# Optimization experiments

Hardware: AMD Instinct MI355X
Metric: run time of the kernel (lower is better)

## Reference

```python
import jax, jax.numpy as jnp
import numpy as np

N, B, D, Q = 32, 36, 2048, 1024  # batch, objects, v_dim, q_dim


def setup_inputs() -> dict:
    key = jax.random.key(0)
    ks = jax.random.split(key, 6)
    sc = 0.02  # small init so ReLU chains stay well-scaled
    return {
        "v": jax.random.normal(ks[0], (N, B, D), jnp.float32),
        "q": jax.random.normal(ks[1], (N, Q), jnp.float32),
        "W1": jax.random.normal(ks[2], (D, D), jnp.float32) * sc,
        "b1": jnp.zeros((D,), jnp.float32),
        "W2": jax.random.normal(ks[3], (D, D), jnp.float32) * sc,
        "b2": jnp.zeros((D,), jnp.float32),
        "W3": jax.random.normal(ks[4], (Q, D), jnp.float32) * sc,
        "b3": jnp.zeros((D,), jnp.float32),
    }


def reference(v, q, W1, b1, W2, b2, W3, b3):
    # FCNet = ReLU(Linear(.)) with weight-norm folded, dropout=0 (eval).
    # Original calls linear3 twice (linear4 unused bug), so q_emb == q_emb2.
    qe = jax.nn.relu(q @ W3 + b3)  # (N, D)
    # pairs[n,i,j] = v[n,i]*qe[n] + v[n,j]*qe[n]  -> (N, B, B, D)
    pairs = (v[:, :, None, :] + v[:, None, :, :]) * qe[:, None, None, :]
    h = jax.nn.relu(jnp.einsum('nijd,de->nije', pairs, W1) + b1)  # linear1
    x = jnp.sum(h, axis=2)  # sum over j relations -> (N, B, D)
    return jax.nn.relu(x @ W2 + b2)  # linear2
```

## Files before the change

kernel.cpp:

```cpp
#include <hip/hip_runtime.h>
#include <stdint.h>

#define N_BATCH 32
#define B_OBJ   36
#define D_DIM   2048
#define Q_DIM   1024

typedef __bf16 bf16x8 __attribute__((ext_vector_type(8)));
typedef float  f32x4  __attribute__((ext_vector_type(4)));

__device__ __forceinline__ uint16_t f2bf(float f) {
    uint32_t u = __builtin_bit_cast(uint32_t, f);
    uint32_t r = (u + 0x7FFFu + ((u >> 16) & 1u)) >> 16;
    return (uint16_t)r;
}

__device__ __forceinline__ void gld_lds16(const void* g, void* l) {
    __builtin_amdgcn_global_load_lds(
        (const __attribute__((address_space(1))) uint32_t*)g,
        (__attribute__((address_space(3))) uint32_t*)l, 16, 0, 0);
}

__global__ __launch_bounds__(256) void transpose_all(
    const float* __restrict__ W1, const float* __restrict__ W2,
    const float* __restrict__ W3,
    uint16_t* __restrict__ W1t, uint16_t* __restrict__ W2t,
    uint16_t* __restrict__ W3t) {
    __shared__ float tile[64][65];
    int gy = blockIdx.y;
    const float* W; uint16_t* Wt; int K, k0;
    if (gy < 32)      { W = W1; Wt = W1t; K = 2048; k0 = gy * 64; }
    else if (gy < 64) { W = W2; Wt = W2t; K = 2048; k0 = (gy - 32) * 64; }
    else              { W = W3; Wt = W3t; K = 1024; k0 = (gy - 64) * 64; }
    int n0 = blockIdx.x * 64;
    int t = threadIdx.x;
    {
        int r = t >> 4, c = (t & 15) * 4;
#pragma unroll
        for (int p = 0; p < 4; ++p)
            *(float4*)&tile[r + p * 16][c] =
                *(const float4*)&W[(size_t)(k0 + r + p * 16) * 2048 + n0 + c];
    }
    __syncthreads();
    {
        int n = t >> 2, kb = (t & 3) * 16;
#pragma unroll
        for (int g4 = 0; g4 < 4; ++g4) {
            int k = kb + g4 * 4;
            ushort4 o;
            o.x = f2bf(tile[k][n]);     o.y = f2bf(tile[k + 1][n]);
            o.z = f2bf(tile[k + 2][n]); o.w = f2bf(tile[k + 3][n]);
            *(ushort4*)&Wt[(size_t)(n0 + n) * K + k0 + k] = o;
        }
    }
}

__global__ __launch_bounds__(256) void qk_gemm(
    const float* __restrict__ q,
    const uint16_t* __restrict__ W3t,
    float* __restrict__ qpart) {
    __shared__ __align__(16) uint16_t As[32][32];
    __shared__ __align__(16) uint16_t Bs[128][32];
    int t = threadIdx.x, lane = t & 63, wave = t >> 6;
    int l15 = lane & 15, quad = lane >> 4;
    int n0 = blockIdx.x * 128;
    int kbase = blockIdx.y * 256;
    f32x4 acc[2][2] = {};
    int ar = t >> 3, ac = (t & 7) * 4;
    int br = t >> 2, bk = (t & 3) * 8;

    for (int k0 = 0; k0 < 256; k0 += 32) {
        __syncthreads();
        float4 av = *(const float4*)&q[(size_t)ar * Q_DIM + kbase + k0 + ac];
        ushort4 a4;
        a4.x = f2bf(av.x); a4.y = f2bf(av.y); a4.z = f2bf(av.z); a4.w = f2bf(av.w);
        *(ushort4*)&As[ar][ac] = a4;
        *(uint4*)&Bs[br][bk]      = *(const uint4*)&W3t[(size_t)(n0 + br) * Q_DIM + kbase + k0 + bk];
        *(uint4*)&Bs[br + 64][bk] = *(const uint4*)&W3t[(size_t)(n0 + br + 64) * Q_DIM + kbase + k0 + bk];
        __syncthreads();
        bf16x8 af[2], bfr[2];
        af[0]  = *(const bf16x8*)&As[l15][quad * 8];
        af[1]  = *(const bf16x8*)&As[16 + l15][quad * 8];
        bfr[0] = *(const bf16x8*)&Bs[wave * 32 + l15][quad * 8];
        bfr[1] = *(const bf16x8*)&Bs[wave * 32 + 16 + l15][quad * 8];
#pragma unroll
        for (int i = 0; i < 2; ++i)
#pragma unroll
            for (int j = 0; j < 2; ++j)
                acc[i][j] = __builtin_amdgcn_mfma_f32_16x16x32_bf16(af[i], bfr[j], acc[i][j], 0, 0, 0);
    }
    float* dst = qpart + (size_t)blockIdx.y * 32 * D_DIM;
#pragma unroll
    for (int i = 0; i < 2; ++i)
#pragma unroll
        for (int j = 0; j < 2; ++j) {
            int n = n0 + wave * 32 + j * 16 + l15;
#pragma unroll
            for (int r = 0; r < 4; ++r)
                dst[(size_t)(i * 16 + quad * 4 + r) * D_DIM + n] = acc[i][j][r];
        }
}

__global__ __launch_bounds__(128) void qe_make_u(
    const float* __restrict__ qpart, const float* __restrict__ b3,
    const float* __restrict__ v, uint16_t* __restrict__ u) {
    int nb = blockIdx.y;
    int d4 = blockIdx.x * 128 + threadIdx.x;
    const float4* p = (const float4*)qpart;
    size_t base = (size_t)nb * 512 + d4;
    float4 s0 = p[base], s1 = p[16384 + base], s2 = p[32768 + base], s3 = p[49152 + base];
    float4 b = ((const float4*)b3)[d4];
    float4 qe;
    qe.x = fmaxf(s0.x + s1.x + s2.x + s3.x + b.x, 0.f);
    qe.y = fmaxf(s0.y + s1.y + s2.y + s3.y + b.y, 0.f);
    qe.z = fmaxf(s0.z + s1.z + s2.z + s3.z + b.z, 0.f);
    qe.w = fmaxf(s0.w + s1.w + s2.w + s3.w + b.w, 0.f);
    const float4* v4 = (const float4*)v;
    ushort4* u4 = (ushort4*)u;
    size_t rb = (size_t)nb * B_OBJ * 512 + d4;
#pragma unroll 4
    for (int i = 0; i < B_OBJ; ++i) {
        float4 vv = v4[rb + (size_t)i * 512];
        ushort4 o;
        o.x = f2bf(vv.x * qe.x);
        o.y = f2bf(vv.y * qe.y);
        o.z = f2bf(vv.z * qe.z);
        o.w = f2bf(vv.w * qe.w);
        u4[rb + (size_t)i * 512] = o;
    }
}

__global__ __launch_bounds__(512) void gemm_batch(
    const uint16_t* __restrict__ A,
    const uint16_t* __restrict__ Bt,
    const float* __restrict__ bias,
    void* __restrict__ Cv,
    int mode) {
    __shared__ __align__(16) uint16_t smem[2][14336];
    float* yt = (float*)&smem[0][0];

    int t = threadIdx.x, lane = t & 63, wave = t >> 6;
    int l15 = lane & 15, quad = lane >> 4;
    int wr = wave >> 2, wc = wave & 3;
    int nbp = blockIdx.y;
    int n0 = blockIdx.x * 128;
    const uint16_t* Ab = A + (size_t)nbp * 72 * D_DIM;

    const uint16_t* gp[4];
    int loff[4];
    int wslot = (lane & 3) ^ ((lane >> 2) & 3);
#pragma unroll
    for (int c = 0; c < 4; ++c) {
        int r = wave + 8 * c;
        int rr = (r < 28) ? r : 0;
        if (rr < 12) {
            int g = rr >> 1, h = rr & 1;
            int arow = g * 16 + (lane >> 2) - (g >= 3 ? 12 : 0);
            gp[c] = Ab + (size_t)arow * D_DIM + h * 32 + wslot * 8;
            loff[c] = h * 3072 + g * 512;
        } else {
            int rb = rr - 12, g = rb >> 1, h = rb & 1;
            int brow = g * 16 + (lane >> 2);
            gp[c] = Bt + (size_t)(n0 + brow) * D_DIM + h * 32 + wslot * 8;
            loff[c] = 6144 + h * 4096 + g * 512;
        }
    }

    f32x4 acc[3][2] = {};
    int rslot = quad ^ (l15 & 3);

#define STAGE(kk, bi)                                    \
    {                                                    \
        _Pragma("unroll")                                \
        for (int c = 0; c < 4; ++c)                      \
            if (wave + 8 * c < 28)                       \
                gld_lds16(gp[c] + (kk), &smem[bi][loff[c]]); \
    }
#define WAIT_L()                                                      \
    {                                                                 \
        if (wave < 4) asm volatile("s_waitcnt vmcnt(4)" ::: "memory");\
        else          asm volatile("s_waitcnt vmcnt(3)" ::: "memory");\
    }

    STAGE(0, 0);
    STAGE(64, 1);
    WAIT_L();
    __builtin_amdgcn_s_barrier();

    for (int k = 0; k < 32; ++k) {
        int cur = k & 1;
        const uint16_t* As = &smem[cur][0];
        const uint16_t* Bs = As + 6144;
#pragma unroll
        for (int s = 0; s < 2; ++s) {
            bf16x8 af[3], bfr[2];
#pragma unroll
            for (int i = 0; i < 3; ++i)
                af[i] = *(const bf16x8*)(As + s * 3072 + (wr * 48 + i * 16 + l15) * 32 + rslot * 8);
#pragma unroll
            for (int j = 0; j < 2; ++j)
                bfr[j] = *(const bf16x8*)(Bs + s * 4096 + (wc * 32 + j * 16 + l15) * 32 + rslot * 8);
#pragma unroll
            for (int i = 0; i < 3; ++i)
#pragma unroll
                for (int j = 0; j < 2; ++j)
                    acc[i][j] = __builtin_amdgcn_mfma_f32_16x16x32_bf16(af[i], bfr[j], acc[i][j], 0, 0, 0);
        }
        if (k == 31) break;
        __builtin_amdgcn_s_barrier();
        if (k < 30) {
            STAGE((k + 2) * 64, cur);
            WAIT_L();
        } else {
            asm volatile("s_waitcnt vmcnt(0)" ::: "memory");
        }
        __builtin_amdgcn_s_barrier();
    }
#undef STAGE
#undef WAIT_L

    if (mode == 0) {
        uint16_t* X = (uint16_t*)Cv;
        __syncthreads();
#pragma unroll
        for (int i = 0; i < 3; ++i)
#pragma unroll
            for (int j = 0; j < 2; ++j)
#pragma unroll
                for (int r = 0; r < 4; ++r)
                    yt[(wr * 48 + i * 16 + quad * 4 + r) * 132 + wc * 32 + j * 16 + l15] = acc[i][j][r];
        __syncthreads();
        int col = t & 127, sub = t >> 7;
        int b = sub >> 1, half = sub & 1;
        float bv = bias[n0 + col];
        float z[36];
#pragma unroll
        for (int j = 0; j < 36; ++j) z[j] = yt[(b * 48 + j) * 132 + col];
#pragma unroll
        for (int ii = 0; ii < 18; ++ii) {
            int i = half * 18 + ii;
            float zi = z[i] + bv;
            float s = 0.f;
#pragma unroll
            for (int j = 0; j < 36; ++j) s += fmaxf(zi + z[j], 0.f);
            X[(size_t)((nbp * 2 + b) * B_OBJ + i) * D_DIM + n0 + col] = f2bf(s);
        }
    } else {
        float* O = (float*)Cv;
#pragma unroll
        for (int i = 0; i < 3; ++i)
#pragma unroll
            for (int r = 0; r < 4; ++r) {
                int obj = i * 16 + quad * 4 + r;
                if (obj < B_OBJ) {
#pragma unroll
                    for (int j = 0; j < 2; ++j) {
                        int cc = n0 + wc * 32 + j * 16 + l15;
                        O[(size_t)((nbp * 2 + wr) * B_OBJ + obj) * D_DIM + cc] =
                            fmaxf(acc[i][j][r] + bias[cc], 0.f);
                    }
                }
            }
    }
}

extern "C" void kernel_launch(void* const* d_in, const int* in_sizes, int n_in,
                              void* d_out, int out_size, void* d_ws, size_t ws_size,
                              hipStream_t stream) {
    const float* v  = (const float*)d_in[0];
    const float* q  = (const float*)d_in[1];
    const float* W1 = (const float*)d_in[2];
    const float* b1 = (const float*)d_in[3];
    const float* W2 = (const float*)d_in[4];
    const float* b2 = (const float*)d_in[5];
    const float* W3 = (const float*)d_in[6];
    const float* b3 = (const float*)d_in[7];
    float* out = (float*)d_out;

    char* ws = (char*)d_ws;
    uint16_t* W1t   = (uint16_t*)(ws + 0);
    uint16_t* W2t   = (uint16_t*)(ws + 8388608);
    uint16_t* W3t   = (uint16_t*)(ws + 16777216);
    uint16_t* u     = (uint16_t*)(ws + 16777216);
    float*    qpart = (float*)   (ws + 21495808);
    uint16_t* x     = (uint16_t*)(ws + 22806528);

    transpose_all<<<dim3(32, 80), 256, 0, stream>>>(W1, W2, W3, W1t, W2t, W3t);

    qk_gemm<<<dim3(16, 4), 256, 0, stream>>>(q, W3t, qpart);

    qe_make_u<<<dim3(4, N_BATCH), 128, 0, stream>>>(qpart, b3, v, u);

    gemm_batch<<<dim3(16, 16), 512, 0, stream>>>(u, W1t, b1, x, 0);

    gemm_batch<<<dim3(16, 16), 512, 0, stream>>>(x, W2t, b2, out, 1);
}
```

Baseline: 171.9 us.

## Fuse all five stages into one cooperative persistent kernel with grid syncs

Replaces the five separate launches (weight transpose/convert, q GEMM, qe/u build, and two batched GEMMs) with one cooperative kernel of 256 blocks. Grid-wide barriers separate the stages. The weight transpose runs as a grid-stride loop, with two 256-thread halves per block each using their own shared-memory tile. The goal is to remove per-launch overhead and the idle gaps between kernels. In exchange it adds grid.sync costs and fixes the grid at 256×512 threads for every phase, so the small stages leave most blocks idle.

Result: slower. 305.7 us (+77.8%).

```diff
diff --git a/kernel.cpp b/kernel.cpp
--- a/kernel.cpp
+++ b/kernel.cpp
@@ -1,5 +1,8 @@
 #include <hip/hip_runtime.h>
+#include <hip/hip_cooperative_groups.h>
 #include <stdint.h>
+
+namespace cg = cooperative_groups;
 
 #define N_BATCH 32
 #define B_OBJ   36
@@ -21,129 +24,16 @@
         (__attribute__((address_space(3))) uint32_t*)l, 16, 0, 0);
 }
 
-__global__ __launch_bounds__(256) void transpose_all(
-    const float* __restrict__ W1, const float* __restrict__ W2,
-    const float* __restrict__ W3,
-    uint16_t* __restrict__ W1t, uint16_t* __restrict__ W2t,
-    uint16_t* __restrict__ W3t) {
-    __shared__ float tile[64][65];
-    int gy = blockIdx.y;
-    const float* W; uint16_t* Wt; int K, k0;
-    if (gy < 32)      { W = W1; Wt = W1t; K = 2048; k0 = gy * 64; }
-    else if (gy < 64) { W = W2; Wt = W2t; K = 2048; k0 = (gy - 32) * 64; }
-    else              { W = W3; Wt = W3t; K = 1024; k0 = (gy - 64) * 64; }
-    int n0 = blockIdx.x * 64;
-    int t = threadIdx.x;
-    {
-        int r = t >> 4, c = (t & 15) * 4;
-#pragma unroll
-        for (int p = 0; p < 4; ++p)
-            *(float4*)&tile[r + p * 16][c] =
-                *(const float4*)&W[(size_t)(k0 + r + p * 16) * 2048 + n0 + c];
-    }
-    __syncthreads();
-    {
-        int n = t >> 2, kb = (t & 3) * 16;
-#pragma unroll
-        for (int g4 = 0; g4 < 4; ++g4) {
-            int k = kb + g4 * 4;
-            ushort4 o;
-            o.x = f2bf(tile[k][n]);     o.y = f2bf(tile[k + 1][n]);
-            o.z = f2bf(tile[k + 2][n]); o.w = f2bf(tile[k + 3][n]);
-            *(ushort4*)&Wt[(size_t)(n0 + n) * K + k0 + k] = o;
-        }
-    }
-}
-
-__global__ __launch_bounds__(256) void qk_gemm(
-    const float* __restrict__ q,
-    const uint16_t* __restrict__ W3t,
-    float* __restrict__ qpart) {
-    __shared__ __align__(16) uint16_t As[32][32];
-    __shared__ __align__(16) uint16_t Bs[128][32];
-    int t = threadIdx.x, lane = t & 63, wave = t >> 6;
-    int l15 = lane & 15, quad = lane >> 4;
-    int n0 = blockIdx.x * 128;
-    int kbase = blockIdx.y * 256;
-    f32x4 acc[2][2] = {};
-    int ar = t >> 3, ac = (t & 7) * 4;
-    int br = t >> 2, bk = (t & 3) * 8;
-
-    for (int k0 = 0; k0 < 256; k0 += 32) {
-        __syncthreads();
-        float4 av = *(const float4*)&q[(size_t)ar * Q_DIM + kbase + k0 + ac];
-        ushort4 a4;
-        a4.x = f2bf(av.x); a4.y = f2bf(av.y); a4.z = f2bf(av.z); a4.w = f2bf(av.w);
-        *(ushort4*)&As[ar][ac] = a4;
-        *(uint4*)&Bs[br][bk]      = *(const uint4*)&W3t[(size_t)(n0 + br) * Q_DIM + kbase + k0 + bk];
-        *(uint4*)&Bs[br + 64][bk] = *(const uint4*)&W3t[(size_t)(n0 + br + 64) * Q_DIM + kbase + k0 + bk];
-        __syncthreads();
-        bf16x8 af[2], bfr[2];
-        af[0]  = *(const bf16x8*)&As[l15][quad * 8];
-        af[1]  = *(const bf16x8*)&As[16 + l15][quad * 8];
-        bfr[0] = *(const bf16x8*)&Bs[wave * 32 + l15][quad * 8];
-        bfr[1] = *(const bf16x8*)&Bs[wave * 32 + 16 + l15][quad * 8];
-#pragma unroll
-        for (int i = 0; i < 2; ++i)
-#pragma unroll
-            for (int j = 0; j < 2; ++j)
-                acc[i][j] = __builtin_amdgcn_mfma_f32_16x16x32_bf16(af[i], bfr[j], acc[i][j], 0, 0, 0);
-    }
-    float* dst = qpart + (size_t)blockIdx.y * 32 * D_DIM;
-#pragma unroll
-    for (int i = 0; i < 2; ++i)
-#pragma unroll
-        for (int j = 0; j < 2; ++j) {
-            int n = n0 + wave * 32 + j * 16 + l15;
-#pragma unroll
-            for (int r = 0; r < 4; ++r)
-                dst[(size_t)(i * 16 + quad * 4 + r) * D_DIM + n] = acc[i][j][r];
-        }
-}
-
-__global__ __launch_bounds__(128) void qe_make_u(
-    const float* __restrict__ qpart, const float* __restrict__ b3,
-    const float* __restrict__ v, uint16_t* __restrict__ u) {
-    int nb = blockIdx.y;
-    int d4 = blockIdx.x * 128 + threadIdx.x;
-    const float4* p = (const float4*)qpart;
-    size_t base = (size_t)nb * 512 + d4;
-    float4 s0 = p[base], s1 = p[16384 + base], s2 = p[32768 + base], s3 = p[49152 + base];
-    float4 b = ((const float4*)b3)[d4];
-    float4 qe;
-    qe.x = fmaxf(s0.x + s1.x + s2.x + s3.x + b.x, 0.f);
-    qe.y = fmaxf(s0.y + s1.y + s2.y + s3.y + b.y, 0.f);
-    qe.z = fmaxf(s0.z + s1.z + s2.z + s3.z + b.z, 0.f);
-    qe.w = fmaxf(s0.w + s1.w + s2.w + s3.w + b.w, 0.f);
-    const float4* v4 = (const float4*)v;
-    ushort4* u4 = (ushort4*)u;
-    size_t rb = (size_t)nb * B_OBJ * 512 + d4;
-#pragma unroll 4
-    for (int i = 0; i < B_OBJ; ++i) {
-        float4 vv = v4[rb + (size_t)i * 512];
-        ushort4 o;
-        o.x = f2bf(vv.x * qe.x);
-        o.y = f2bf(vv.y * qe.y);
-        o.z = f2bf(vv.z * qe.z);
-        o.w = f2bf(vv.w * qe.w);
-        u4[rb + (size_t)i * 512] = o;
-    }
-}
-
-__global__ __launch_bounds__(512) void gemm_batch(
-    const uint16_t* __restrict__ A,
-    const uint16_t* __restrict__ Bt,
-    const float* __restrict__ bias,
-    void* __restrict__ Cv,
-    int mode) {
-    __shared__ __align__(16) uint16_t smem[2][14336];
+__device__ __forceinline__ void gemm_phase(
+    const uint16_t* A, const uint16_t* Bt, const float* bias, void* Cv,
+    int mode, uint16_t (*smem)[14336], int t, int bid) {
     float* yt = (float*)&smem[0][0];
 
-    int t = threadIdx.x, lane = t & 63, wave = t >> 6;
+    int lane = t & 63, wave = t >> 6;
     int l15 = lane & 15, quad = lane >> 4;
     int wr = wave >> 2, wc = wave & 3;
-    int nbp = blockIdx.y;
-    int n0 = blockIdx.x * 128;
+    int nbp = bid >> 4;
+    int n0 = (bid & 15) * 128;
     const uint16_t* Ab = A + (size_t)nbp * 72 * D_DIM;
 
     const uint16_t* gp[4];
@@ -264,6 +154,137 @@
     }
 }
 
+__global__ __launch_bounds__(512) void fused_all(
+    const float* __restrict__ v, const float* __restrict__ q,
+    const float* __restrict__ W1, const float* __restrict__ b1,
+    const float* __restrict__ W2, const float* __restrict__ b2,
+    const float* __restrict__ W3, const float* __restrict__ b3,
+    float* __restrict__ out,
+    uint16_t* W1t, uint16_t* W2t, uint16_t* W3t,
+    uint16_t* u, float* qpart, uint16_t* x) {
+    __shared__ __align__(16) uint16_t smem[2][14336];
+    int t = threadIdx.x;
+    int bid = blockIdx.x;
+    cg::grid_group grid = cg::this_grid();
+
+    {
+        int half = t >> 8, tt = t & 255;
+        float (*tile)[65] = (float(*)[65])(&smem[0][0] + half * 8320);
+        for (int vb = bid * 2 + half; vb < 2560; vb += 512) {
+            int gy = vb >> 5, n0 = (vb & 31) * 64;
+            const float* W; uint16_t* Wt; int K, k0;
+            if (gy < 32)      { W = W1; Wt = W1t; K = 2048; k0 = gy * 64; }
+            else if (gy < 64) { W = W2; Wt = W2t; K = 2048; k0 = (gy - 32) * 64; }
+            else              { W = W3; Wt = W3t; K = 1024; k0 = (gy - 64) * 64; }
+            {
+                int r = tt >> 4, c = (tt & 15) * 4;
+#pragma unroll
+                for (int p = 0; p < 4; ++p)
+                    *(float4*)&tile[r + p * 16][c] =
+                        *(const float4*)&W[(size_t)(k0 + r + p * 16) * 2048 + n0 + c];
+            }
+            __syncthreads();
+            {
+                int n = tt >> 2, kb = (tt & 3) * 16;
+#pragma unroll
+                for (int g4 = 0; g4 < 4; ++g4) {
+                    int k = kb + g4 * 4;
+                    ushort4 o;
+                    o.x = f2bf(tile[k][n]);     o.y = f2bf(tile[k + 1][n]);
+                    o.z = f2bf(tile[k + 2][n]); o.w = f2bf(tile[k + 3][n]);
+                    *(ushort4*)&Wt[(size_t)(n0 + n) * K + k0 + k] = o;
+                }
+            }
+            __syncthreads();
+        }
+    }
+    grid.sync();
+
+    {
+        int half = t >> 8, tt = t & 255;
+        int vb = bid * 2 + half;
+        if (vb < 64) {
+            uint16_t* As = &smem[0][0] + half * 5120;
+            uint16_t* Bs = As + 1024;
+            int lane = tt & 63, wave = tt >> 6;
+            int l15 = lane & 15, quad = lane >> 4;
+            int n0 = (vb & 15) * 128;
+            int kbase = (vb >> 4) * 256;
+            f32x4 acc[2][2] = {};
+            int ar = tt >> 3, ac = (tt & 7) * 4;
+            int br = tt >> 2, bk = (tt & 3) * 8;
+            for (int k0 = 0; k0 < 256; k0 += 32) {
+                __syncthreads();
+                float4 av = *(const float4*)&q[(size_t)ar * Q_DIM + kbase + k0 + ac];
+                ushort4 a4;
+                a4.x = f2bf(av.x); a4.y = f2bf(av.y); a4.z = f2bf(av.z); a4.w = f2bf(av.w);
+                *(ushort4*)&As[ar * 32 + ac] = a4;
+                *(uint4*)&Bs[br * 32 + bk] =
+                    *(const uint4*)&W3t[(size_t)(n0 + br) * Q_DIM + kbase + k0 + bk];
+                *(uint4*)&Bs[(br + 64) * 32 + bk] =
+                    *(const uint4*)&W3t[(size_t)(n0 + br + 64) * Q_DIM + kbase + k0 + bk];
+                __syncthreads();
+                bf16x8 af[2], bfr[2];
+                af[0]  = *(const bf16x8*)&As[l15 * 32 + quad * 8];
+                af[1]  = *(const bf16x8*)&As[(16 + l15) * 32 + quad * 8];
+                bfr[0] = *(const bf16x8*)&Bs[(wave * 32 + l15) * 32 + quad * 8];
+                bfr[1] = *(const bf16x8*)&Bs[(wave * 32 + 16 + l15) * 32 + quad * 8];
+#pragma unroll
+                for (int i = 0; i < 2; ++i)
+#pragma unroll
+                    for (int j = 0; j < 2; ++j)
+                        acc[i][j] = __builtin_amdgcn_mfma_f32_16x16x32_bf16(af[i], bfr[j], acc[i][j], 0, 0, 0);
+            }
+            float* dst = qpart + (size_t)(vb >> 4) * 32 * D_DIM;
+#pragma unroll
+            for (int i = 0; i < 2; ++i)
+#pragma unroll
+                for (int j = 0; j < 2; ++j) {
+                    int n = n0 + wave * 32 + j * 16 + l15;
+#pragma unroll
+                    for (int r = 0; r < 4; ++r)
+                        dst[(size_t)(i * 16 + quad * 4 + r) * D_DIM + n] = acc[i][j][r];
+                }
+        }
+    }
+    grid.sync();
+
+    {
+        int idx = bid * 512 + t;
+        if (idx < 16384) {
+            int nb = idx >> 9, d4 = idx & 511;
+            const float4* p = (const float4*)qpart;
+            size_t base = (size_t)nb * 512 + d4;
+            float4 s0 = p[base], s1 = p[16384 + base], s2 = p[32768 + base], s3 = p[49152 + base];
+            float4 b = ((const float4*)b3)[d4];
+            float4 qe;
+            qe.x = fmaxf(s0.x + s1.x + s2.x + s3.x + b.x, 0.f);
+            qe.y = fmaxf(s0.y + s1.y + s2.y + s3.y + b.y, 0.f);
+            qe.z = fmaxf(s0.z + s1.z + s2.z + s3.z + b.z, 0.f);
+            qe.w = fmaxf(s0.w + s1.w + s2.w + s3.w + b.w, 0.f);
+            const float4* v4 = (const float4*)v;
+            ushort4* u4 = (ushort4*)u;
+            size_t rb = (size_t)nb * B_OBJ * 512 + d4;
+#pragma unroll 4
+            for (int i = 0; i < B_OBJ; ++i) {
+                float4 vv = v4[rb + (size_t)i * 512];
+                ushort4 o;
+                o.x = f2bf(vv.x * qe.x);
+                o.y = f2bf(vv.y * qe.y);
+                o.z = f2bf(vv.z * qe.z);
+                o.w = f2bf(vv.w * qe.w);
+                u4[rb + (size_t)i * 512] = o;
+            }
+        }
+    }
+    grid.sync();
+
+    gemm_phase(u, W1t, b1, x, 0, smem, t, bid);
+    grid.sync();
+
+    gemm_phase(x, W2t, b2, out, 1, smem, t, bid);
+}
+
 extern "C" void kernel_launch(void* const* d_in, const int* in_sizes, int n_in,
                               void* d_out, int out_size, void* d_ws, size_t ws_size,
                               hipStream_t stream) {
@@ -285,13 +306,10 @@
     float*    qpart = (float*)   (ws + 21495808);
     uint16_t* x     = (uint16_t*)(ws + 22806528);
 
-    transpose_all<<<dim3(32, 80), 256, 0, stream>>>(W1, W2, W3, W1t, W2t, W3t);
-
-    qk_gemm<<<dim3(16, 4), 256, 0, stream>>>(q, W3t, qpart);
-
-    qe_make_u<<<dim3(4, N_BATCH), 128, 0, stream>>>(qpart, b3, v, u);
-
-    gemm_batch<<<dim3(16, 16), 512, 0, stream>>>(u, W1t, b1, x, 0);
-
-    gemm_batch<<<dim3(16, 16), 512, 0, stream>>>(x, W2t, b2, out, 1);
-}
+    void* args[] = {
+        (void*)&v, (void*)&q, (void*)&W1, (void*)&b1, (void*)&W2, (void*)&b2,
+        (void*)&W3, (void*)&b3, (void*)&out, (void*)&W1t, (void*)&W2t,
+        (void*)&W3t, (void*)&u, (void*)&qpart, (void*)&x};
+    hipLaunchCooperativeKernel((const void*)fused_all, dim3(256), dim3(512),
+                               args, 0, stream);
+}
```
